# Kernel tuning notes

Measured on AMD Instinct MI355X. Metric: run time of the kernel, lower is better.

The kernel has to match this reference:

```python
import jax, jax.numpy as jnp
import numpy as np

B, T, N = 32, 720, 321
K = 25        # moving-average kernel_size (init kwarg)
DEC_LEV = 3   # wavelet decomposition level (init kwarg)
F = 16        # sym8 filter length
A = 0.85      # soft-threshold shrink factor from the source

# pywt sym8 decomposition low-pass filter
_DEC_LO = np.array([
    -0.0033824159510061256, -0.00054213233179114812, 0.031695087811492981,
    0.0076074873249176054, -0.14329423835080971, -0.061273359067658524,
    0.48135965125837221, 0.77718575170052351, 0.36444189483533893,
    -0.051945838107709037, -0.027219029917056003, 0.049137179673607506,
    0.0038087520138906151, -0.014952258337048231, -0.0003029205147213668,
    0.0018899503327594609], dtype=np.float32)
_DEC_HI = (((-1.0) ** (np.arange(F) + 1)) * _DEC_LO[::-1]).astype(np.float32)
DEC_LO = jnp.asarray(_DEC_LO)
DEC_HI = jnp.asarray(_DEC_HI)
REC_LO = DEC_LO[::-1]
REC_HI = DEC_HI[::-1]


def _dwt(a):
    # single-level DWT, pywt 'symmetric' extension, downsample odd phase
    ext = jnp.pad(a, (F - 1, F - 1), mode='symmetric')
    ca = jnp.convolve(ext, DEC_LO, mode='valid')[1::2]
    cd = jnp.convolve(ext, DEC_HI, mode='valid')[1::2]
    return ca, cd


def _idwt(ca, cd):
    # upsample (zeros in odd slots), full conv with reconstruction filters, trim F-2
    L = ca.shape[0]
    up_a = jnp.zeros(2 * L - 1, ca.dtype).at[::2].set(ca)
    up_d = jnp.zeros(2 * L - 1, cd.dtype).at[::2].set(cd)
    rec = jnp.convolve(up_a, REC_LO) + jnp.convolve(up_d, REC_HI)
    return rec[F - 2: rec.shape[0] - (F - 2)]


def _denoise(sig):
    # wavedec -> universal soft-threshold (shrunk by A) on all detail levels -> waverec
    L = sig.shape[0]
    a = sig
    details = []  # details[0] = finest level cD1
    for _ in range(DEC_LEV):
        a, d = _dwt(a)
        details.append(d)
    sigma = jnp.median(jnp.abs(details[0])) / 0.6745
    lam = sigma * jnp.sqrt(jnp.float32(2.0 * np.log(float(L))))
    details = [jnp.where(jnp.abs(d) >= lam,
                         jnp.sign(d) * (jnp.abs(d) - A * lam),
                         jnp.zeros_like(d)) for d in details]
    for d in reversed(details):
        if a.shape[0] == d.shape[0] + 1:  # static-shape pywt length fixup
            a = a[:-1]
        a = _idwt(a, d)
    return a


def _moving_avg(x):
    # replicate-pad (K-1)//2 on both ends of time axis, then AvgPool1d(K, stride=1)
    p = (K - 1) // 2
    xp = jnp.concatenate([jnp.repeat(x[:, :1], p, axis=1), x,
                          jnp.repeat(x[:, -1:], p, axis=1)], axis=1)
    s = jax.lax.reduce_window(xp, 0.0, jax.lax.add, (1, K, 1), (1, 1, 1), 'VALID')
    return s / K


def _forward(x):
    trend = _moving_avg(x)            # [B,T,N]
    res = x - trend
    # T is even so the odd-length branch of the original is never taken
    trend_nn = _denoise(trend.reshape(-1)).reshape(x.shape)
    res_nn = _denoise(res.reshape(-1)).reshape(x.shape)
    return trend - trend_nn, trend_nn, res - res_nn, res_nn


def setup_inputs() -> dict:
    key = jax.random.key(0)
    return {"x": jax.random.normal(key, (B, T, N), dtype=jnp.float32)}


def reference(x):
    return _forward(x)
```

## Files before the change

kernel.cpp:

```cpp
#include <hip/hip_runtime.h>
#include <math.h>

#define BB 32
#define TT 720
#define NNN 321
#define KK 25
#define PP 12
#define TCH 24

constexpr int L0 = BB * TT * NNN;
constexpr int L1 = (L0 + 15) / 2;
constexpr int L2 = (L1 + 15) / 2;
constexpr int L3 = (L2 + 15) / 2;
constexpr unsigned KMED = (unsigned)((L1 - 1) / 2 + 1);
constexpr float AA = 0.85f;

constexpr int NH1B = 512;
constexpr int CH   = (L1 + NH1B - 1) / NH1B;
constexpr int CANDSZ = NH1B * CH;

#define NC3 1024
constexpr int LEN2T = 2 * NC3 + 32;
constexpr int LEN1T = 4 * NC3 + 80;
#define NF0 4096
constexpr int N1T = NF0 / 2 + 8;
constexpr int N2T = N1T / 2 + 7;
constexpr int NQ3 = (N2T + 1) / 2;

constexpr float DLO[16] = {
    -0.0033824159510061256f, -0.0005421323317911481f, 0.03169508781149298f,
    0.007607487324917605f,  -0.1432942383508097f,    -0.061273359067658524f,
    0.4813596512583722f,     0.7771857517005235f,     0.36444189483533895f,
    -0.05194583810770904f,  -0.027219029917056003f,   0.049137179673607506f,
    0.003808752013890615f,  -0.01495225833704823f,   -0.0003029205147213668f,
    0.0018899503327594609f };

__device__ void select_body(unsigned* hist, unsigned* prefix, unsigned* kArr,
                            float* lamArr, int nbins, int shift) {
    int t = threadIdx.x;
    int chunk = nbins >> 8;
    __shared__ unsigned wsum[4];
    for (int s = 0; s < 2; ++s) {
        unsigned loc[16];
        unsigned* hs = hist + s * 4096 + t * chunk;
        unsigned csum = 0;
        for (int j = 0; j < chunk; ++j) { loc[j] = atomicExch(&hs[j], 0u); csum += loc[j]; }
        unsigned v = csum;
        int lane = t & 63, wv = t >> 6;
#pragma unroll
        for (int off = 1; off < 64; off <<= 1) {
            unsigned u = (unsigned)__shfl_up((int)v, off, 64);
            if (lane >= off) v += u;
        }
        if (lane == 63) wsum[wv] = v;
        __syncthreads();
        unsigned base = 0;
        for (int w2 = 0; w2 < wv; ++w2) base += wsum[w2];
        unsigned incl = base + v, excl = incl - csum;
        unsigned k = kArr[s];
        if (excl < k && incl >= k) {
            unsigned run = excl;
            for (int j = 0; j < chunk; ++j) {
                if (run < k && run + loc[j] >= k) {
                    unsigned digit = (unsigned)(t * chunk + j);
                    unsigned npref = prefix[s] | (digit << shift);
                    prefix[s] = npref;
                    kArr[s] = k - run;
                    if (shift == 0) {
                        float med = __uint_as_float(npref);
                        lamArr[s] = (med / 0.6745f) * sqrtf(2.0f * logf((float)L0));
                    }
                    break;
                }
                run += loc[j];
            }
        }
        __syncthreads();
    }
}

__device__ bool i_am_last(unsigned* done, unsigned nBlocks) {
    __shared__ int amLast;
    __syncthreads();
    if (threadIdx.x == 0) {
        unsigned prev = atomicAdd(done, 1u);
        amLast = (prev == nBlocks - 1) ? 1 : 0;
    }
    __syncthreads();
    return amLast != 0;
}

__global__ void mavg_kernel(const float* __restrict__ x,
                            float* __restrict__ trend,
                            float* __restrict__ res,
                            unsigned* __restrict__ hist,
                            unsigned* __restrict__ prefix,
                            unsigned* __restrict__ kArr,
                            unsigned* __restrict__ done) {
    constexpr int NCH = TT / TCH;
    int gid = blockIdx.x * blockDim.x + threadIdx.x;
    if (gid < 8192) hist[gid] = 0;
    if (gid < 2) { prefix[gid] = 0; kArr[gid] = KMED; }
    if (gid < 3) done[gid] = 0;
    if (gid >= BB * NCH * NNN) return;
    int n    = gid % NNN;
    int rest = gid / NNN;
    int ch   = rest % NCH;
    int b    = rest / NCH;
    int t0   = ch * TCH;
    const float* xb = x + (size_t)b * TT * NNN + n;
    float sum = 0.f;
#pragma unroll
    for (int dt = -PP; dt <= PP; ++dt) {
        int tt = t0 + dt;
        tt = tt < 0 ? 0 : (tt >= TT ? TT - 1 : tt);
        sum += xb[(size_t)tt * NNN];
    }
    size_t base = (size_t)b * TT * NNN + (size_t)t0 * NNN + n;
    for (int i = 0; i < TCH; ++i) {
        int t = t0 + i;
        float tr = sum * (1.0f / (float)KK);
        size_t idx = base + (size_t)i * NNN;
        trend[idx] = tr;
        res[idx] = xb[(size_t)t * NNN] - tr;
        int tp = t + 1 + PP; if (tp > TT - 1) tp = TT - 1;
        int tm = t - PP;     if (tm < 0)      tm = 0;
        sum += xb[(size_t)tp * NNN] - xb[(size_t)tm * NNN];
    }
}

__global__ void dwt123_kernel(const float* __restrict__ trend,
                              const float* __restrict__ res,
                              float* __restrict__ cd1,
                              float* __restrict__ cd2,
                              float* __restrict__ ca3,
                              float* __restrict__ cd3,
                              unsigned* __restrict__ hist,
                              unsigned* __restrict__ prefix,
                              unsigned* __restrict__ kArr,
                              float* __restrict__ lamArr,
                              unsigned* __restrict__ done) {
    int s = blockIdx.y;
    int C0 = blockIdx.x * NC3;
    const float* a0 = s ? res : trend;
    __shared__ float s1[LEN1T];
    __shared__ float s2[LEN2T];
    __shared__ unsigned sh[4096];
    for (int b = threadIdx.x; b < 4096; b += 256) sh[b] = 0;
    __syncthreads();

    int T0 = 2 * C0 - 14;
    int S1 = 4 * C0 - 42; if (S1 < 0) S1 = 0;
    int E1 = 2 * (T0 + LEN2T) + 2; if (E1 > L1) E1 = L1;
    int len1 = E1 - S1;
    float* pcd1 = cd1 + (size_t)s * L1;

    int npair = (len1 + 1) / 2;
    for (int ip = threadIdx.x; ip < npair; ip += 256) {
        int i = 2 * ip;
        int o = S1 + i;
        float slo0, shi0, slo1, shi1;
        if (2 * o - 14 >= 0 && 2 * o + 3 < L0) {
            const float* p = a0 + 2 * o - 14;
            float v[18];
#pragma unroll
            for (int j = 0; j < 18; ++j) v[j] = p[j];
            slo0 = shi0 = slo1 = shi1 = 0.f;
#pragma unroll
            for (int j = 0; j < 16; ++j) {
                float h = (j & 1) ? DLO[15 - j] : -DLO[15 - j];
                slo0 = fmaf(DLO[j], v[15 - j], slo0);
                shi0 = fmaf(h,      v[15 - j], shi0);
                slo1 = fmaf(DLO[j], v[17 - j], slo1);
                shi1 = fmaf(h,      v[17 - j], shi1);
            }
        } else {
            float acc[2][2];
#pragma unroll
            for (int q = 0; q < 2; ++q) {
                int oo = o + q;
                float slo = 0.f, shi = 0.f;
                int bidx = 2 * oo + 1;
#pragma unroll
                for (int j = 0; j < 16; ++j) {
                    int idx = bidx - j;
                    if (idx < 0) idx = -1 - idx;
                    if (idx >= L0) idx = 2 * L0 - 1 - idx;
                    float v = a0[idx];
                    slo = fmaf(DLO[j], v, slo);
                    float h = (j & 1) ? DLO[15 - j] : -DLO[15 - j];
                    shi = fmaf(h, v, shi);
                }
                acc[q][0] = slo; acc[q][1] = shi;
            }
            slo0 = acc[0][0]; shi0 = acc[0][1];
            slo1 = acc[1][0]; shi1 = acc[1][1];
        }
        s1[i] = slo0;
        if (o >= 4 * C0 && o < 4 * C0 + 4 * NC3) {
            pcd1[o] = shi0;
            atomicAdd(&sh[__float_as_uint(fabsf(shi0)) >> 20], 1u);
        }
        if (i + 1 < len1) {
            s1[i + 1] = slo1;
            int o1 = o + 1;
            if (o1 >= 4 * C0 && o1 < 4 * C0 + 4 * NC3) {
                pcd1[o1] = shi1;
                atomicAdd(&sh[__float_as_uint(fabsf(shi1)) >> 20], 1u);
            }
        }
    }
    __syncthreads();

    for (int b = threadIdx.x; b < 4096; b += 256) {
        unsigned c = sh[b];
        if (c) atomicAdd(&hist[s * 4096 + b], c);
    }

    float* pcd2 = cd2 + (size_t)s * L2;
    for (int i = threadIdx.x; i < LEN2T; i += 256) {
        int e = T0 + i;
        if (e < 0 || e >= L2) continue;
        int base = 2 * e + 1;
        float slo = 0.f, shi = 0.f;
#pragma unroll
        for (int j = 0; j < 16; ++j) {
            int idx = base - j;
            if (idx < 0) idx = -1 - idx;
            if (idx >= L1) idx = 2 * L1 - 1 - idx;
            float v = s1[idx - S1];
            slo = fmaf(DLO[j], v, slo);
            float h = (j & 1) ? DLO[15 - j] : -DLO[15 - j];
            shi = fmaf(h, v, shi);
        }
        s2[i] = slo;
        if (e >= 2 * C0 && e < 2 * C0 + 2 * NC3) pcd2[e] = shi;
    }
    __syncthreads();
    for (int i = threadIdx.x; i < LEN2T; i += 256) {
        int e = T0 + i;
        if (e < 0)        s2[i] = s2[(-1 - e) - T0];
        else if (e >= L2) s2[i] = s2[(2 * L2 - 1 - e) - T0];
    }
    __syncthreads();
    float* pca3 = ca3 + (size_t)s * L3;
    float* pcd3 = cd3 + (size_t)s * L3;
    for (int i = threadIdx.x; i < NC3; i += 256) {
        int o = C0 + i;
        if (o >= L3) break;
        int b2 = 2 * o + 1 - T0;
        float slo = 0.f, shi = 0.f;
#pragma unroll
        for (int j = 0; j < 16; ++j) {
            float v = s2[b2 - j];
            slo = fmaf(DLO[j], v, slo);
            float h = (j & 1) ? DLO[15 - j] : -DLO[15 - j];
            shi = fmaf(h, v, shi);
        }
        pca3[o] = slo;
        pcd3[o] = shi;
    }

    if (i_am_last(done + 0, gridDim.x * gridDim.y))
        select_body(hist, prefix, kArr, lamArr, 4096, 20);
}

__device__ __forceinline__ float sthr(float d, float lam, float alam) {
    float ad = fabsf(d);
    return (ad >= lam) ? copysignf(ad - alam, d) : 0.f;
}

__global__ void idwt_fused(const float* __restrict__ ca3,
                           const float* __restrict__ cd3,
                           const float* __restrict__ cd2,
                           const float* __restrict__ cd1,
                           const float* __restrict__ trend,
                           const float* __restrict__ res,
                           float* __restrict__ out,
                           const float* __restrict__ lamArr) {
    int s = blockIdx.y;
    int F0 = blockIdx.x * NF0;
    float lam = lamArr[s], alam = AA * lam;
    const float* pa3 = ca3 + (size_t)s * L3;
    const float* pd3 = cd3 + (size_t)s * L3;
    const float* pd2 = cd2 + (size_t)s * L2;
    const float* pd1 = cd1 + (size_t)s * L1;
    __shared__ float r2[N2T + 1];
    __shared__ float r1[N1T];
    int A1 = F0 >> 1, A2 = F0 >> 2, Q3 = F0 >> 3;
    for (int i = threadIdx.x; i < NQ3; i += 256) {
        int q3 = Q3 + i;
        float a0 = 0.f, a1 = 0.f;
#pragma unroll
        for (int p = 0; p < 8; ++p) {
            int idx = q3 + p; if (idx > L3 - 1) idx = L3 - 1;
            float a = pa3[idx];
            float d = sthr(pd3[idx], lam, alam);
            a0 = fmaf(a, DLO[2 * p + 1], a0);
            a0 = fmaf(d, DLO[14 - 2 * p], a0);
            a1 = fmaf(a, DLO[2 * p], a1);
            a1 = fmaf(d, -DLO[15 - 2 * p], a1);
        }
        r2[2 * i] = a0; r2[2 * i + 1] = a1;
    }
    __syncthreads();
    for (int i = threadIdx.x; i < N1T / 2; i += 256) {
        int q2 = A2 + i;
        float a0 = 0.f, a1 = 0.f;
#pragma unroll
        for (int p = 0; p < 8; ++p) {
            float a = r2[i + p];
            int idx = q2 + p; if (idx > L2 - 1) idx = L2 - 1;
            float d = sthr(pd2[idx], lam, alam);
            a0 = fmaf(a, DLO[2 * p + 1], a0);
            a0 = fmaf(d, DLO[14 - 2 * p], a0);
            a1 = fmaf(a, DLO[2 * p], a1);
            a1 = fmaf(d, -DLO[15 - 2 * p], a1);
        }
        r1[2 * i] = a0; r1[2 * i + 1] = a1;
    }
    __syncthreads();
    const float* orig = s ? res : trend;
    float* o_diff = out + (size_t)(2 * s) * L0;
    float* o_nn   = out + (size_t)(2 * s + 1) * L0;
    for (int i = threadIdx.x; i < NF0 / 4; i += 256) {
        int ii = 2 * i;
        int q1 = A1 + ii;
        int r0 = 2 * q1;
        if (r0 >= L0) break;
        float d[9];
#pragma unroll
        for (int p = 0; p < 9; ++p) {
            int idx = q1 + p; if (idx > L1 - 1) idx = L1 - 1;
            d[p] = sthr(pd1[idx], lam, alam);
        }
        float a0 = 0.f, a1 = 0.f, b0 = 0.f, b1 = 0.f;
#pragma unroll
        for (int p = 0; p < 8; ++p) {
            float a  = r1[ii + p];
            float ab = r1[ii + 1 + p];
            a0 = fmaf(a,      DLO[2 * p + 1], a0);
            a0 = fmaf(d[p],   DLO[14 - 2 * p], a0);
            a1 = fmaf(a,      DLO[2 * p], a1);
            a1 = fmaf(d[p],  -DLO[15 - 2 * p], a1);
            b0 = fmaf(ab,     DLO[2 * p + 1], b0);
            b0 = fmaf(d[p+1], DLO[14 - 2 * p], b0);
            b1 = fmaf(ab,     DLO[2 * p], b1);
            b1 = fmaf(d[p+1],-DLO[15 - 2 * p], b1);
        }
        float4 o4 = *(const float4*)(orig + r0);
        float4 nn; nn.x = a0; nn.y = a1; nn.z = b0; nn.w = b1;
        float4 df; df.x = o4.x - a0; df.y = o4.y - a1; df.z = o4.z - b0; df.w = o4.w - b1;
        *(float4*)(o_nn + r0)   = nn;
        *(float4*)(o_diff + r0) = df;
    }
}

__global__ void hist1_kernel(const float* __restrict__ d,
                             unsigned* __restrict__ hist,
                             unsigned* __restrict__ prefix,
                             unsigned* __restrict__ cand,
                             unsigned* __restrict__ bcnt,
                             unsigned* __restrict__ kArr,
                             float* __restrict__ lamArr,
                             unsigned* __restrict__ done) {
    int s = blockIdx.y;
    int blk = blockIdx.x;
    const float* ds = d + (size_t)s * L1;
    unsigned* cs = cand + (size_t)s * CANDSZ + (size_t)blk * CH;
    __shared__ unsigned sh[4096];
    __shared__ unsigned slocal;
    for (int b = threadIdx.x; b < 4096; b += 256) sh[b] = 0;
    if (threadIdx.x == 0) slocal = 0;
    __syncthreads();
    unsigned pref = prefix[s] >> 20;
    int i0 = blk * CH;
    int i1 = i0 + CH; if (i1 > L1) i1 = L1;
    for (int i = i0 + threadIdx.x; i < i1; i += 256) {
        unsigned u = __float_as_uint(fabsf(ds[i]));
        if ((u >> 20) == pref) {
            atomicAdd(&sh[(u >> 8) & 0xFFFu], 1u);
            unsigned pos = atomicAdd(&slocal, 1u);
            cs[pos] = u;
        }
    }
    __syncthreads();
    if (threadIdx.x == 0) bcnt[s * NH1B + blk] = slocal;
    for (int b = threadIdx.x; b < 4096; b += 256) {
        unsigned c = sh[b];
        if (c) atomicAdd(&hist[s * 4096 + b], c);
    }
    if (i_am_last(done + 1, gridDim.x * gridDim.y))
        select_body(hist, prefix, kArr, lamArr, 4096, 8);
}

__global__ void hist2_kernel(const unsigned* __restrict__ cand,
                             unsigned* __restrict__ hist,
                             unsigned* __restrict__ prefix,
                             const unsigned* __restrict__ bcnt,
                             unsigned* __restrict__ kArr,
                             float* __restrict__ lamArr,
                             unsigned* __restrict__ done) {
    int s = blockIdx.y;
    int blk = blockIdx.x;
    const unsigned* cs = cand + (size_t)s * CANDSZ + (size_t)blk * CH;
    __shared__ unsigned sh[256];
    sh[threadIdx.x] = 0;
    __syncthreads();
    unsigned pref = prefix[s] >> 8;
    unsigned n = bcnt[s * NH1B + blk];
    for (unsigned i = threadIdx.x; i < n; i += 256) {
        unsigned u = cs[i];
        if ((u >> 8) == pref) atomicAdd(&sh[u & 0xFFu], 1u);
    }
    __syncthreads();
    unsigned c = sh[threadIdx.x];
    if (c) atomicAdd(&hist[s * 4096 + threadIdx.x], c);
    if (i_am_last(done + 2, gridDim.x * gridDim.y))
        select_body(hist, prefix, kArr, lamArr, 256, 0);
}

extern "C" void kernel_launch(void* const* d_in, const int* in_sizes, int n_in,
                              void* d_out, int out_size, void* d_ws, size_t ws_size,
                              hipStream_t stream) {
    const float* x = (const float*)d_in[0];
    float* out = (float*)d_out;
    float* w = (float*)d_ws;

    float* trend = w;
    float* res   = w + (size_t)L0;
    float* cd1   = w + 2 * (size_t)L0;
    float* cd2   = cd1 + 2 * (size_t)L1;
    float* ca3   = cd2 + 2 * (size_t)L2;
    float* cd3   = ca3 + 2 * (size_t)L3;
    unsigned* cand   = (unsigned*)(cd3 + 2 * (size_t)L3);
    unsigned* hist   = cand + 2 * (size_t)CANDSZ;
    unsigned* prefix = hist + 8192;
    unsigned* kArr   = prefix + 2;
    float*    lamArr = (float*)(kArr + 2);
    unsigned* bcnt   = (unsigned*)(lamArr + 2);
    unsigned* done   = bcnt + 2 * NH1B;

    dim3 b256(256);

    {
        int nthreads = BB * (TT / TCH) * NNN;
        mavg_kernel<<<(nthreads + 255) / 256, b256, 0, stream>>>(
            x, trend, res, hist, prefix, kArr, done);
    }
    dwt123_kernel<<<dim3((L3 + NC3 - 1) / NC3, 2), b256, 0, stream>>>(
        trend, res, cd1, cd2, ca3, cd3, hist, prefix, kArr, lamArr, done);
    hist1_kernel<<<dim3(NH1B, 2), b256, 0, stream>>>(
        cd1, hist, prefix, cand, bcnt, kArr, lamArr, done);
    hist2_kernel<<<dim3(NH1B, 2), b256, 0, stream>>>(
        cand, hist, prefix, bcnt, kArr, lamArr, done);
    idwt_fused<<<dim3((L0 + NF0 - 1) / NF0, 2), b256, 0, stream>>>(
        ca3, cd3, cd2, cd1, trend, res, out, lamArr);
}
```

Before: 329.1 us.

## Vectorize DWT loads/stores, pad coefficient arrays, and rebalance radix-select histogram bits

```diff
diff --git a/kernel.cpp b/kernel.cpp
--- a/kernel.cpp
+++ b/kernel.cpp
@@ -12,6 +12,9 @@
 constexpr int L1 = (L0 + 15) / 2;
 constexpr int L2 = (L1 + 15) / 2;
 constexpr int L3 = (L2 + 15) / 2;
+constexpr int L1P = L1 + 1;
+constexpr int L2P = L2 + 1;
+constexpr int L3P = L3 + 1;
 constexpr unsigned KMED = (unsigned)((L1 - 1) / 2 + 1);
 constexpr float AA = 0.85f;
 
@@ -145,34 +148,36 @@
     const float* a0 = s ? res : trend;
     __shared__ float s1[LEN1T];
     __shared__ float s2[LEN2T];
-    __shared__ unsigned sh[4096];
-    for (int b = threadIdx.x; b < 4096; b += 256) sh[b] = 0;
+    unsigned* shst = (unsigned*)s2;
+
+    for (int b = threadIdx.x; b < 2048; b += 256) shst[b] = 0;
     __syncthreads();
 
     int T0 = 2 * C0 - 14;
     int S1 = 4 * C0 - 42; if (S1 < 0) S1 = 0;
     int E1 = 2 * (T0 + LEN2T) + 2; if (E1 > L1) E1 = L1;
     int len1 = E1 - S1;
-    float* pcd1 = cd1 + (size_t)s * L1;
+    float* pcd1 = cd1 + (size_t)s * L1P;
 
     int npair = (len1 + 1) / 2;
     for (int ip = threadIdx.x; ip < npair; ip += 256) {
         int i = 2 * ip;
         int o = S1 + i;
         float slo0, shi0, slo1, shi1;
-        if (2 * o - 14 >= 0 && 2 * o + 3 < L0) {
-            const float* p = a0 + 2 * o - 14;
-            float v[18];
-#pragma unroll
-            for (int j = 0; j < 18; ++j) v[j] = p[j];
+        if (2 * o - 16 >= 0 && 2 * o + 3 < L0) {
+            const float4* p4 = (const float4*)(a0 + 2 * o - 16);
+            float4 qa = p4[0], qb = p4[1], qc = p4[2], qd = p4[3], qe = p4[4];
+            float v[20] = { qa.x,qa.y,qa.z,qa.w, qb.x,qb.y,qb.z,qb.w,
+                            qc.x,qc.y,qc.z,qc.w, qd.x,qd.y,qd.z,qd.w,
+                            qe.x,qe.y,qe.z,qe.w };
             slo0 = shi0 = slo1 = shi1 = 0.f;
 #pragma unroll
             for (int j = 0; j < 16; ++j) {
                 float h = (j & 1) ? DLO[15 - j] : -DLO[15 - j];
-                slo0 = fmaf(DLO[j], v[15 - j], slo0);
-                shi0 = fmaf(h,      v[15 - j], shi0);
-                slo1 = fmaf(DLO[j], v[17 - j], slo1);
-                shi1 = fmaf(h,      v[17 - j], shi1);
+                slo0 = fmaf(DLO[j], v[17 - j], slo0);
+                shi0 = fmaf(h,      v[17 - j], shi0);
+                slo1 = fmaf(DLO[j], v[19 - j], slo1);
+                shi1 = fmaf(h,      v[19 - j], shi1);
             }
         } else {
             float acc[2][2];
@@ -197,44 +202,72 @@
             slo1 = acc[1][0]; shi1 = acc[1][1];
         }
         s1[i] = slo0;
+        if (i + 1 < len1) s1[i + 1] = slo1;
         if (o >= 4 * C0 && o < 4 * C0 + 4 * NC3) {
-            pcd1[o] = shi0;
-            atomicAdd(&sh[__float_as_uint(fabsf(shi0)) >> 20], 1u);
-        }
-        if (i + 1 < len1) {
-            s1[i + 1] = slo1;
-            int o1 = o + 1;
-            if (o1 >= 4 * C0 && o1 < 4 * C0 + 4 * NC3) {
-                pcd1[o1] = shi1;
-                atomicAdd(&sh[__float_as_uint(fabsf(shi1)) >> 20], 1u);
-            }
-        }
-    }
-    __syncthreads();
-
-    for (int b = threadIdx.x; b < 4096; b += 256) {
-        unsigned c = sh[b];
+            unsigned u0 = __float_as_uint(fabsf(shi0));
+            if (i + 1 < len1) {
+                *(float2*)(pcd1 + o) = make_float2(shi0, shi1);
+                unsigned u1 = __float_as_uint(fabsf(shi1));
+                atomicAdd(&shst[u0 >> 21], 1u);
+                atomicAdd(&shst[u1 >> 21], 1u);
+            } else {
+                pcd1[o] = shi0;
+                atomicAdd(&shst[u0 >> 21], 1u);
+            }
+        }
+    }
+    __syncthreads();
+
+    for (int b = threadIdx.x; b < 2048; b += 256) {
+        unsigned c = shst[b];
         if (c) atomicAdd(&hist[s * 4096 + b], c);
     }
-
-    float* pcd2 = cd2 + (size_t)s * L2;
-    for (int i = threadIdx.x; i < LEN2T; i += 256) {
-        int e = T0 + i;
-        if (e < 0 || e >= L2) continue;
-        int base = 2 * e + 1;
-        float slo = 0.f, shi = 0.f;
-#pragma unroll
-        for (int j = 0; j < 16; ++j) {
-            int idx = base - j;
-            if (idx < 0) idx = -1 - idx;
-            if (idx >= L1) idx = 2 * L1 - 1 - idx;
-            float v = s1[idx - S1];
-            slo = fmaf(DLO[j], v, slo);
-            float h = (j & 1) ? DLO[15 - j] : -DLO[15 - j];
-            shi = fmaf(h, v, shi);
-        }
-        s2[i] = slo;
-        if (e >= 2 * C0 && e < 2 * C0 + 2 * NC3) pcd2[e] = shi;
+    __syncthreads();
+
+    float* pcd2 = cd2 + (size_t)s * L2P;
+    for (int ip = threadIdx.x; ip < LEN2T / 2; ip += 256) {
+        int i0 = 2 * ip;
+        int e0 = T0 + i0;
+        int e1 = e0 + 1;
+        if (2 * e0 - 14 >= 0 && 2 * e1 + 1 < L1 && e1 < L2) {
+            const float2* wp2 = (const float2*)(s1 + (2 * e0 - 14 - S1));
+            float w[18];
+#pragma unroll
+            for (int j = 0; j < 9; ++j) { float2 t2 = wp2[j]; w[2*j] = t2.x; w[2*j+1] = t2.y; }
+            float slo0 = 0.f, shi0 = 0.f, slo1 = 0.f, shi1 = 0.f;
+#pragma unroll
+            for (int j = 0; j < 16; ++j) {
+                float h = (j & 1) ? DLO[15 - j] : -DLO[15 - j];
+                slo0 = fmaf(DLO[j], w[15 - j], slo0);
+                shi0 = fmaf(h,      w[15 - j], shi0);
+                slo1 = fmaf(DLO[j], w[17 - j], slo1);
+                shi1 = fmaf(h,      w[17 - j], shi1);
+            }
+            s2[i0] = slo0; s2[i0 + 1] = slo1;
+            if (e0 >= 2 * C0 && e0 < 2 * C0 + 2 * NC3)
+                *(float2*)(pcd2 + e0) = make_float2(shi0, shi1);
+        } else {
+#pragma unroll
+            for (int q = 0; q < 2; ++q) {
+                int i = i0 + q;
+                int e = T0 + i;
+                if (e < 0 || e >= L2) continue;
+                int base = 2 * e + 1;
+                float slo = 0.f, shi = 0.f;
+#pragma unroll
+                for (int j = 0; j < 16; ++j) {
+                    int idx = base - j;
+                    if (idx < 0) idx = -1 - idx;
+                    if (idx >= L1) idx = 2 * L1 - 1 - idx;
+                    float v = s1[idx - S1];
+                    slo = fmaf(DLO[j], v, slo);
+                    float h = (j & 1) ? DLO[15 - j] : -DLO[15 - j];
+                    shi = fmaf(h, v, shi);
+                }
+                s2[i] = slo;
+                if (e >= 2 * C0 && e < 2 * C0 + 2 * NC3) pcd2[e] = shi;
+            }
+        }
     }
     __syncthreads();
     for (int i = threadIdx.x; i < LEN2T; i += 256) {
@@ -243,26 +276,35 @@
         else if (e >= L2) s2[i] = s2[(2 * L2 - 1 - e) - T0];
     }
     __syncthreads();
-    float* pca3 = ca3 + (size_t)s * L3;
-    float* pcd3 = cd3 + (size_t)s * L3;
-    for (int i = threadIdx.x; i < NC3; i += 256) {
-        int o = C0 + i;
-        if (o >= L3) break;
-        int b2 = 2 * o + 1 - T0;
-        float slo = 0.f, shi = 0.f;
+    float* pca3 = ca3 + (size_t)s * L3P;
+    float* pcd3 = cd3 + (size_t)s * L3P;
+    for (int ip = threadIdx.x; ip < NC3 / 2; ip += 256) {
+        int i0 = 2 * ip;
+        int o0 = C0 + i0;
+        if (o0 >= L3) break;
+        const float2* wp2 = (const float2*)(s2 + i0 * 2);
+        float w[18];
+#pragma unroll
+        for (int j = 0; j < 9; ++j) { float2 t2 = wp2[j]; w[2*j] = t2.x; w[2*j+1] = t2.y; }
+        float slo0 = 0.f, shi0 = 0.f, slo1 = 0.f, shi1 = 0.f;
 #pragma unroll
         for (int j = 0; j < 16; ++j) {
-            float v = s2[b2 - j];
-            slo = fmaf(DLO[j], v, slo);
             float h = (j & 1) ? DLO[15 - j] : -DLO[15 - j];
-            shi = fmaf(h, v, shi);
-        }
-        pca3[o] = slo;
-        pcd3[o] = shi;
+            slo0 = fmaf(DLO[j], w[15 - j], slo0);
+            shi0 = fmaf(h,      w[15 - j], shi0);
+            slo1 = fmaf(DLO[j], w[17 - j], slo1);
+            shi1 = fmaf(h,      w[17 - j], shi1);
+        }
+        if (o0 + 1 < L3) {
+            *(float2*)(pca3 + o0) = make_float2(slo0, slo1);
+            *(float2*)(pcd3 + o0) = make_float2(shi0, shi1);
+        } else {
+            pca3[o0] = slo0; pcd3[o0] = shi0;
+        }
     }
 
     if (i_am_last(done + 0, gridDim.x * gridDim.y))
-        select_body(hist, prefix, kArr, lamArr, 4096, 20);
+        select_body(hist, prefix, kArr, lamArr, 2048, 21);
 }
 
 __device__ __forceinline__ float sthr(float d, float lam, float alam) {
@@ -281,10 +323,10 @@
     int s = blockIdx.y;
     int F0 = blockIdx.x * NF0;
     float lam = lamArr[s], alam = AA * lam;
-    const float* pa3 = ca3 + (size_t)s * L3;
-    const float* pd3 = cd3 + (size_t)s * L3;
-    const float* pd2 = cd2 + (size_t)s * L2;
-    const float* pd1 = cd1 + (size_t)s * L1;
+    const float* pa3 = ca3 + (size_t)s * L3P;
+    const float* pd3 = cd3 + (size_t)s * L3P;
+    const float* pd2 = cd2 + (size_t)s * L2P;
+    const float* pd1 = cd1 + (size_t)s * L1P;
     __shared__ float r2[N2T + 1];
     __shared__ float r1[N1T];
     int A1 = F0 >> 1, A2 = F0 >> 2, Q3 = F0 >> 3;
@@ -329,10 +371,20 @@
         int r0 = 2 * q1;
         if (r0 >= L0) break;
         float d[9];
-#pragma unroll
-        for (int p = 0; p < 9; ++p) {
-            int idx = q1 + p; if (idx > L1 - 1) idx = L1 - 1;
-            d[p] = sthr(pd1[idx], lam, alam);
+        if (q1 + 9 <= L1) {
+            const float2* pp = (const float2*)(pd1 + q1);
+            float2 e0 = pp[0], e1 = pp[1], e2 = pp[2], e3 = pp[3];
+            d[0] = sthr(e0.x, lam, alam); d[1] = sthr(e0.y, lam, alam);
+            d[2] = sthr(e1.x, lam, alam); d[3] = sthr(e1.y, lam, alam);
+            d[4] = sthr(e2.x, lam, alam); d[5] = sthr(e2.y, lam, alam);
+            d[6] = sthr(e3.x, lam, alam); d[7] = sthr(e3.y, lam, alam);
+            d[8] = sthr(pd1[q1 + 8], lam, alam);
+        } else {
+#pragma unroll
+            for (int p = 0; p < 9; ++p) {
+                int idx = q1 + p; if (idx > L1 - 1) idx = L1 - 1;
+                d[p] = sthr(pd1[idx], lam, alam);
+            }
         }
         float a0 = 0.f, a1 = 0.f, b0 = 0.f, b1 = 0.f;
 #pragma unroll
@@ -366,20 +418,20 @@
                              unsigned* __restrict__ done) {
     int s = blockIdx.y;
     int blk = blockIdx.x;
-    const float* ds = d + (size_t)s * L1;
+    const float* ds = d + (size_t)s * L1P;
     unsigned* cs = cand + (size_t)s * CANDSZ + (size_t)blk * CH;
     __shared__ unsigned sh[4096];
     __shared__ unsigned slocal;
     for (int b = threadIdx.x; b < 4096; b += 256) sh[b] = 0;
     if (threadIdx.x == 0) slocal = 0;
     __syncthreads();
-    unsigned pref = prefix[s] >> 20;
+    unsigned pref = prefix[s] >> 21;
     int i0 = blk * CH;
     int i1 = i0 + CH; if (i1 > L1) i1 = L1;
     for (int i = i0 + threadIdx.x; i < i1; i += 256) {
         unsigned u = __float_as_uint(fabsf(ds[i]));
-        if ((u >> 20) == pref) {
-            atomicAdd(&sh[(u >> 8) & 0xFFFu], 1u);
+        if ((u >> 21) == pref) {
+            atomicAdd(&sh[(u >> 9) & 0xFFFu], 1u);
             unsigned pos = atomicAdd(&slocal, 1u);
             cs[pos] = u;
         }
@@ -391,7 +443,7 @@
         if (c) atomicAdd(&hist[s * 4096 + b], c);
     }
     if (i_am_last(done + 1, gridDim.x * gridDim.y))
-        select_body(hist, prefix, kArr, lamArr, 4096, 8);
+        select_body(hist, prefix, kArr, lamArr, 4096, 9);
 }
 
 __global__ void hist2_kernel(const unsigned* __restrict__ cand,
@@ -404,20 +456,22 @@
     int s = blockIdx.y;
     int blk = blockIdx.x;
     const unsigned* cs = cand + (size_t)s * CANDSZ + (size_t)blk * CH;
-    __shared__ unsigned sh[256];
-    sh[threadIdx.x] = 0;
-    __syncthreads();
-    unsigned pref = prefix[s] >> 8;
+    __shared__ unsigned sh[512];
+    sh[threadIdx.x] = 0; sh[threadIdx.x + 256] = 0;
+    __syncthreads();
+    unsigned pref = prefix[s] >> 9;
     unsigned n = bcnt[s * NH1B + blk];
     for (unsigned i = threadIdx.x; i < n; i += 256) {
         unsigned u = cs[i];
-        if ((u >> 8) == pref) atomicAdd(&sh[u & 0xFFu], 1u);
-    }
-    __syncthreads();
-    unsigned c = sh[threadIdx.x];
-    if (c) atomicAdd(&hist[s * 4096 + threadIdx.x], c);
+        if ((u >> 9) == pref) atomicAdd(&sh[u & 0x1FFu], 1u);
+    }
+    __syncthreads();
+    for (int b = threadIdx.x; b < 512; b += 256) {
+        unsigned c = sh[b];
+        if (c) atomicAdd(&hist[s * 4096 + b], c);
+    }
     if (i_am_last(done + 2, gridDim.x * gridDim.y))
-        select_body(hist, prefix, kArr, lamArr, 256, 0);
+        select_body(hist, prefix, kArr, lamArr, 512, 0);
 }
 
 extern "C" void kernel_launch(void* const* d_in, const int* in_sizes, int n_in,
@@ -430,10 +484,10 @@
     float* trend = w;
     float* res   = w + (size_t)L0;
     float* cd1   = w + 2 * (size_t)L0;
-    float* cd2   = cd1 + 2 * (size_t)L1;
-    float* ca3   = cd2 + 2 * (size_t)L2;
-    float* cd3   = ca3 + 2 * (size_t)L3;
-    unsigned* cand   = (unsigned*)(cd3 + 2 * (size_t)L3);
+    float* cd2   = cd1 + 2 * (size_t)L1P;
+    float* ca3   = cd2 + 2 * (size_t)L2P;
+    float* cd3   = ca3 + 2 * (size_t)L3P;
+    unsigned* cand   = (unsigned*)(cd3 + 2 * (size_t)L3P);
     unsigned* hist   = cand + 2 * (size_t)CANDSZ;
     unsigned* prefix = hist + 8192;
     unsigned* kArr   = prefix + 2;
```

Result: faster. 295.6 us (-10.2%).
